# Optimization experiments

Hardware: AMD Instinct MI355X
Metric: run time of the kernel (lower is better)

The kernel has to match this reference:

```python
import jax, jax.numpy as jnp
from jax import lax
import numpy as np

GRID = 64
MAP = 15000.0
SCALE = MAP / GRID  # 234.375
R = int(1100 / SCALE)  # 4
SIGMA = 1.5
C = 16
B = 768
N_KILL = 49152
N_TRAIL = 393216

TOWERS = np.array([(8955, 8510), (9767, 10113), (11134, 11207), (11593, 11669), (13052, 12612), (12611, 13084), (5846, 6396), (5048, 4812), (3651, 3696), (3210, 3217), (2177, 1807), (1748, 2270), (4318, 13875), (981, 10441), (7943, 13411), (1512, 6699), (1169, 4287), (1172, 3583), (10481, 13650), (11275, 13657), (11275, 13663), (13866, 4505), (10504, 1029), (13327, 8226), (13624, 10572), (6919, 1483), (13599, 11319), (4281, 1253), (3468, 1230), (13594, 11319)], dtype=np.float32)

# ---- static buffers (numpy, computed once at import) ----
_tg = np.clip((TOWERS / SCALE).astype(np.int64), 0, GRID - 1)
TX, TY = _tg[:, 0], _tg[:, 1]
_xs = np.arange(GRID)
# per-tower coverage disc on the full canvas: equivalent to clipped range_mask placement
DISC = (((_xs[None, None, :] - TX[:, None, None]) ** 2 + (_xs[None, :, None] - TY[:, None, None]) ** 2) <= R * R).astype(np.float32)  # [30, H, W]
_ks = int(2 * 4 * SIGMA + 1)
if _ks % 2 == 0:
    _ks += 1
_x = (np.arange(_ks) - _ks // 2).astype(np.float32)
_k1 = np.exp(-_x ** 2 / (2 * SIGMA ** 2))
_k2 = np.outer(_k1, _k1)
_k2 = _k2 / _k2.sum()
KERNEL = np.broadcast_to(_k2, (C, 1, _ks, _ks)).astype(np.float32).copy()  # depthwise OIHW
PAD = _ks // 2
DRAG_X, DRAG_Y = int(10000.0 / SCALE), int(5000.0 / SCALE)   # (42, 21)
BARON_X, BARON_Y = int(5000.0 / SCALE), int(10000.0 / SCALE)  # (21, 42)


def _to_grid(coords):
    return jnp.clip((coords / SCALE).astype(jnp.int32), 0, GRID - 1)


def setup_inputs() -> dict:
    key = jax.random.key(0)
    ks = jax.random.split(key, 10)
    return {
        "player_coords": jax.random.uniform(ks[0], (N_TRAIL, 2), jnp.float32) * MAP,
        "player_vals": jax.random.uniform(ks[1], (N_TRAIL,), jnp.float32),
        "dead_towers_mask": jax.random.uniform(ks[2], (B, 30), jnp.float32),
        "kill_coords": jax.random.uniform(ks[3], (N_KILL, 2), jnp.float32) * MAP,
        "kill_vals": jax.random.uniform(ks[4], (N_KILL,), jnp.float32),
        "obj_status": jax.random.uniform(ks[5], (B, 2), jnp.float32),
        "player_b_idx": jax.random.randint(ks[6], (N_TRAIL,), 0, B, jnp.int32),
        "player_channels": jax.random.randint(ks[7], (N_TRAIL,), 0, 10, jnp.int32),
        "kill_teams": jax.random.randint(ks[8], (N_KILL,), 0, 2, jnp.int32),
        "kill_b_idx": jax.random.randint(ks[9], (N_KILL,), 0, B, jnp.int32),
    }


def reference(player_coords, player_vals, dead_towers_mask, kill_coords, kill_vals, obj_status, player_b_idx, player_channels, kill_teams, kill_b_idx):
    b = dead_towers_mask.shape[0]
    dead = dead_towers_mask > 0.5          # [B, 30]
    alive_f = (~dead).astype(jnp.float32)
    dead_f = dead.astype(jnp.float32)

    # channels 0/1: alive/dead tower markers (idempotent set -> scatter-max)
    ch0 = jnp.zeros((b, GRID, GRID), jnp.float32).at[:, TY, TX].max(alive_f)
    ch1 = jnp.zeros((b, GRID, GRID), jnp.float32).at[:, TY, TX].max(dead_f)

    # channel 2: max of binary range discs over alive towers == any-coverage indicator
    cov = alive_f @ jnp.asarray(DISC).reshape(30, -1)  # [B, H*W]
    ch2 = (cov > 0).astype(jnp.float32).reshape(b, GRID, GRID)

    # channel 3: objective markers
    ch3 = (jnp.zeros((b, GRID, GRID), jnp.float32)
           .at[:, DRAG_Y, DRAG_X].set((obj_status[:, 0] > 0.5).astype(jnp.float32))
           .at[:, BARON_Y, BARON_X].set((obj_status[:, 1] > 0.5).astype(jnp.float32)))

    canvas = jnp.concatenate(
        [ch0[:, None], ch1[:, None], ch2[:, None], ch3[:, None],
         jnp.zeros((b, C - 4, GRID, GRID), jnp.float32)], axis=1)  # [B, 16, H, W]

    # kill events: scatter-add into channels 4 + team
    kg = _to_grid(kill_coords)
    canvas = canvas.at[kill_b_idx, 4 + kill_teams, kg[:, 1], kg[:, 0]].add(kill_vals)

    # player trails: scatter-add into channels 6 + player_channel
    pg = _to_grid(player_coords)
    canvas = canvas.at[player_b_idx, 6 + player_channels, pg[:, 1], pg[:, 0]].add(player_vals)

    # depthwise gaussian blur
    blurred = lax.conv_general_dilated(
        canvas, jnp.asarray(KERNEL),
        window_strides=(1, 1), padding=[(PAD, PAD), (PAD, PAD)],
        feature_group_count=C,
        dimension_numbers=("NCHW", "OIHW", "NCHW"))
    return blurred
```

## Files before the change

### kernel.cpp

```cpp
#include <hip/hip_runtime.h>
#include <string.h>

#define GRID    64
#define BATCH   768
#define C       16
#define NT      30
#define N_KILL  49152
#define N_TRAIL 393216
#define CELLS   4096
#define IMG     (C * CELLS)
#define SCALE   234.375f
#define NSC     12
#define NIMG    (BATCH * NSC)
#define CAPI    128
#define STR     65
#define ROWS    76
#define HWORDS  (ROWS * STR)

__device__ constexpr int TXc[NT] = {38,41,47,49,55,53,24,21,15,13, 9, 7,18, 4,33, 6, 4, 5,44,48,48,59,44,56,58,29,58,18,14,58};
__device__ constexpr int TYc[NT] = {36,43,47,49,53,55,27,20,15,13, 7, 9,59,44,57,28,18,15,58,58,58,19, 4,35,45, 6,48, 5, 5,48};

__device__ constexpr float W13[13] = {
    8.92216e-05f, 1.02820e-03f, 7.59741e-03f, 3.59943e-02f, 1.09341e-01f,
    2.12968e-01f, 2.65964e-01f, 2.12968e-01f, 1.09341e-01f, 3.59943e-02f,
    7.59741e-03f, 1.02820e-03f, 8.92216e-05f};

__global__ __launch_bounds__(256) void zero_counts(unsigned* __restrict__ counts) {
    const int gid = blockIdx.x * 256 + threadIdx.x;
    if (gid < NIMG) counts[gid] = 0;
}

__global__ __launch_bounds__(256) void bin_points(
    const float* __restrict__ kc, const float* __restrict__ kv,
    const int*   __restrict__ kt, const int*   __restrict__ kb,
    const float* __restrict__ pc, const float* __restrict__ pv,
    const int*   __restrict__ pb, const int*   __restrict__ pch,
    unsigned* __restrict__ counts, unsigned* __restrict__ recs)
{
    const int gid = blockIdx.x * 256 + threadIdx.x;
    int img, gx, gy; float val;
    if (gid < N_KILL) {
        const int i = gid;
        const float2 xy = ((const float2*)kc)[i];
        gx = min(max((int)(xy.x / SCALE), 0), GRID - 1);
        gy = min(max((int)(xy.y / SCALE), 0), GRID - 1);
        val = kv[i];
        img = kb[i] * NSC + kt[i];
    } else {
        const int i = gid - N_KILL;
        const float2 xy = ((const float2*)pc)[i];
        gx = min(max((int)(xy.x / SCALE), 0), GRID - 1);
        gy = min(max((int)(xy.y / SCALE), 0), GRID - 1);
        val = pv[i];
        img = pb[i] * NSC + 2 + pch[i];
    }
    _Float16 h = (_Float16)val;
    unsigned short us;
    memcpy(&us, &h, 2);
    const unsigned rec = ((unsigned)(gy * GRID + gx) << 16) | (unsigned)us;
    const unsigned slot = atomicAdd(&counts[img], 1u);
    if (slot < CAPI) recs[(size_t)img * CAPI + slot] = rec;
}

template<bool BINS>
__global__ __launch_bounds__(256) void fused_blur(
    const float* __restrict__ dead_mask,
    const float* __restrict__ obj_status,
    const unsigned* __restrict__ counts,
    const unsigned* __restrict__ recs,
    const float* canvas,
    float* __restrict__ out)
{
    const int t  = threadIdx.x;
    const int bc = blockIdx.x;
    const int b  = bc >> 4;
    const int c  = bc & 15;
    const size_t base = (size_t)bc * CELLS;
    const int u = t & 63, q = t >> 6;

    __shared__ __align__(16) float s_h[HWORDS];
    __shared__ unsigned s_recs[CAPI];
    __shared__ float s_w[13];
    __shared__ float s_alive[NT];

    const bool sparse = (c != 2) && (BINS || c < 4);

    int n = 0;
    if (sparse) {
        if (c >= 4) {
            const int img = b * NSC + (c - 4);
            if (t < CAPI) s_recs[t] = recs[(size_t)img * CAPI + t];
            n = min((int)counts[img], CAPI);
        } else {
            if (t < 32) {
                int gx, gy; unsigned hbits = 0;
                if (t < NT) {
                    gx = TXc[t]; gy = TYc[t];
                    if (c != 3) {
                        const float a  = (dead_mask[b * NT + t] > 0.5f) ? 0.f : 1.f;
                        float v;
                        if (c == 0) {
                            v = (t == 20 || t == 29) ? 0.f
                              : (t == 19) ? fmaxf(a, (dead_mask[b*NT+20] > 0.5f) ? 0.f : 1.f)
                              : (t == 26) ? fmaxf(a, (dead_mask[b*NT+29] > 0.5f) ? 0.f : 1.f)
                              : a;
                        } else {
                            const float d = 1.f - a;
                            v = (t == 20 || t == 29) ? 0.f
                              : (t == 19) ? fmaxf(d, (dead_mask[b*NT+20] > 0.5f) ? 1.f : 0.f)
                              : (t == 26) ? fmaxf(d, (dead_mask[b*NT+29] > 0.5f) ? 1.f : 0.f)
                              : d;
                        }
                        hbits = (v > 0.5f) ? 0x3C00u : 0u;
                    }
                } else {
                    gx = (t == NT) ? 42 : 21;
                    gy = (t == NT) ? 21 : 42;
                    if (c == 3)
                        hbits = (obj_status[b * 2 + (t - NT)] > 0.5f) ? 0x3C00u : 0u;
                }
                s_recs[t] = ((unsigned)(gy * GRID + gx) << 16) | hbits;
            }
            n = 32;
        }
    } else if (c == 2) {
        if (t < NT) s_alive[t] = (dead_mask[b * NT + t] > 0.5f) ? 0.0f : 1.0f;
    }
    if (t < 13) s_w[t] = W13[t];

    {
        float4* z4 = (float4*)s_h;
        const float4 z = make_float4(0.f, 0.f, 0.f, 0.f);
        #pragma unroll
        for (int i = 0; i < 5; ++i) {
            const int idx = i * 256 + t;
            if (idx < HWORDS / 4) z4[idx] = z;
        }
    }
    __syncthreads();

    if (sparse) {
        const int ntaps = n * 13;
        for (int k0 = 0; k0 < ntaps; k0 += 256) {
            const int k = k0 + t;
            int i = (int)((unsigned)k / 13u);
            const int dd = k - i * 13;
            const bool valid = (k < ntaps);
            if (i > n - 1) i = n - 1;

            const unsigned rec = (n > 0) ? s_recs[i] : 0u;
            const int gx = (int)((rec >> 16) & 63u);
            const int gy = (int)(rec >> 22);
            const unsigned short us = (unsigned short)(rec & 0xFFFFu);
            _Float16 h;
            memcpy(&h, &us, 2);
            const float val = (float)h;

            const int   xl = gx - 6 + dd;
            if (valid && (unsigned)xl < 64u && val != 0.f)
                atomicAdd(&s_h[(6 + gy) * STR + xl], s_w[dd] * val);
        }
    } else {
        float w28[28];
        if (c == 2) {
            unsigned long long mask = 0ULL;
            #pragma unroll
            for (int i = 0; i < NT; ++i) {
                const int dy  = u - TYc[i];
                const int ady = dy < 0 ? -dy : dy;
                if (ady <= 4 && s_alive[i] > 0.0f) {
                    const int hw = (ady == 0) ? 4 : (ady <= 2) ? 3 : (ady == 3) ? 2 : 0;
                    int lo = TXc[i] - hw; if (lo < 0)  lo = 0;
                    int hi = TXc[i] + hw; if (hi > 63) hi = 63;
                    mask |= (((1ULL << (hi - lo + 1)) - 1ULL) << lo);
                }
            }
            #pragma unroll
            for (int k = 0; k < 28; ++k) {
                const int col = 16 * q - 6 + k;
                w28[k] = ((unsigned)col < 64u) ? (float)((mask >> col) & 1ULL) : 0.f;
            }
        } else {
            #pragma unroll
            for (int k = 0; k < 28; ++k) {
                const int col = 16 * q - 6 + k;
                w28[k] = ((unsigned)col < 64u) ? canvas[base + u * GRID + col] : 0.f;
            }
        }
        #pragma unroll
        for (int j = 0; j < 16; ++j) {
            float acc = 0.f;
            #pragma unroll
            for (int d = 0; d < 13; ++d) acc = fmaf(W13[d], w28[j + d], acc);
            s_h[(6 + u) * STR + 16 * q + j] = acc;
        }
    }
    __syncthreads();

    float v[28];
    #pragma unroll
    for (int k = 0; k < 28; ++k) v[k] = s_h[(16 * q + k) * STR + u];
    #pragma unroll
    for (int j = 0; j < 16; ++j) {
        float acc = 0.f;
        #pragma unroll
        for (int d = 0; d < 13; ++d) acc = fmaf(W13[d], v[j + d], acc);
        out[base + (16 * q + j) * GRID + u] = acc;
    }
}

__global__ __launch_bounds__(256) void zero12(float* __restrict__ out) {
    const int j = blockIdx.x;
    const int b = j / NSC, ch = 4 + j % NSC;
    float4* p = (float4*)(out + (size_t)(b * C + ch) * CELLS);
    #pragma unroll
    for (int k = 0; k < 4; ++k) p[k * 256 + threadIdx.x] = make_float4(0.f,0.f,0.f,0.f);
}

__global__ __launch_bounds__(256) void scatter_global(
    const float* __restrict__ kc, const float* __restrict__ kv,
    const int*   __restrict__ kt, const int*   __restrict__ kb,
    const float* __restrict__ pc, const float* __restrict__ pv,
    const int*   __restrict__ pb, const int*   __restrict__ pch,
    float* __restrict__ out)
{
    const int gid = blockIdx.x * 256 + threadIdx.x;
    if (gid < N_KILL) {
        const int i = gid;
        const int gx = min(max((int)(kc[2*i]   / SCALE), 0), GRID - 1);
        const int gy = min(max((int)(kc[2*i+1] / SCALE), 0), GRID - 1);
        atomicAdd(out + (size_t)kb[i]*IMG + (4+kt[i])*CELLS + gy*GRID + gx, kv[i]);
    } else {
        const int i = gid - N_KILL;
        const int gx = min(max((int)(pc[2*i]   / SCALE), 0), GRID - 1);
        const int gy = min(max((int)(pc[2*i+1] / SCALE), 0), GRID - 1);
        atomicAdd(out + (size_t)pb[i]*IMG + (6+pch[i])*CELLS + gy*GRID + gx, pv[i]);
    }
}

extern "C" void kernel_launch(void* const* d_in, const int* in_sizes, int n_in,
                              void* d_out, int out_size, void* d_ws, size_t ws_size,
                              hipStream_t stream)
{
    const float* player_coords = (const float*)d_in[0];
    const float* player_vals   = (const float*)d_in[1];
    const float* dead_mask     = (const float*)d_in[2];
    const float* kill_coords   = (const float*)d_in[3];
    const float* kill_vals     = (const float*)d_in[4];
    const float* obj_status    = (const float*)d_in[5];
    const int*   player_b      = (const int*)d_in[6];
    const int*   player_ch     = (const int*)d_in[7];
    const int*   kill_teams    = (const int*)d_in[8];
    const int*   kill_b        = (const int*)d_in[9];
    float* out = (float*)d_out;

    const size_t counts_bytes = (size_t)NIMG * sizeof(unsigned);
    const size_t recs_bytes   = (size_t)NIMG * CAPI * sizeof(unsigned);
    const int n_scatter_blocks = (N_KILL + N_TRAIL) / 256;

    if (ws_size >= counts_bytes + recs_bytes) {
        unsigned* counts = (unsigned*)d_ws;
        unsigned* recs   = (unsigned*)((char*)d_ws + counts_bytes);
        zero_counts<<<(NIMG + 255) / 256, 256, 0, stream>>>(counts);
        bin_points<<<n_scatter_blocks, 256, 0, stream>>>(
            kill_coords, kill_vals, kill_teams, kill_b,
            player_coords, player_vals, player_b, player_ch,
            counts, recs);
        fused_blur<true><<<BATCH * C, 256, 0, stream>>>(
            dead_mask, obj_status, counts, recs, nullptr, out);
    } else {
        zero12<<<NIMG, 256, 0, stream>>>(out);
        scatter_global<<<n_scatter_blocks, 256, 0, stream>>>(
            kill_coords, kill_vals, kill_teams, kill_b,
            player_coords, player_vals, player_b, player_ch, out);
        fused_blur<false><<<BATCH * C, 256, 0, stream>>>(
            dead_mask, obj_status, nullptr, nullptr, out, out);
    }
}
```

Measured before the change: 101.9 us.

## Fuse zero, bin and blur into one cooperative persistent kernel with grid syncs

Replaces the three-kernel sequence (zero counts, bin points, blur) with a single cooperative persistent kernel. It uses grid-wide syncs between the phases and loops over images with a grid-stride. The aim is to remove two kernel launch boundaries and their drain/fill gaps. In exchange it adds host-side occupancy queries on each call, grid.sync overhead, and a grid limited to resident blocks, which may cost blur throughput; if the cooperative launch fails it falls back to the old path.

```diff
diff --git a/kernel.cpp b/kernel.cpp
--- a/kernel.cpp
+++ b/kernel.cpp
@@ -1,5 +1,8 @@
 #include <hip/hip_runtime.h>
+#include <hip/hip_cooperative_groups.h>
 #include <string.h>
+
+namespace cg = cooperative_groups;
 
 #define GRID    64
 #define BATCH   768
@@ -7,6 +10,7 @@
 #define NT      30
 #define N_KILL  49152
 #define N_TRAIL 393216
+#define NPTS    (N_KILL + N_TRAIL)
 #define CELLS   4096
 #define IMG     (C * CELLS)
 #define SCALE   234.375f
@@ -25,63 +29,24 @@
     2.12968e-01f, 2.65964e-01f, 2.12968e-01f, 1.09341e-01f, 3.59943e-02f,
     7.59741e-03f, 1.02820e-03f, 8.92216e-05f};
 
-__global__ __launch_bounds__(256) void zero_counts(unsigned* __restrict__ counts) {
-    const int gid = blockIdx.x * 256 + threadIdx.x;
-    if (gid < NIMG) counts[gid] = 0;
-}
-
-__global__ __launch_bounds__(256) void bin_points(
-    const float* __restrict__ kc, const float* __restrict__ kv,
-    const int*   __restrict__ kt, const int*   __restrict__ kb,
-    const float* __restrict__ pc, const float* __restrict__ pv,
-    const int*   __restrict__ pb, const int*   __restrict__ pch,
-    unsigned* __restrict__ counts, unsigned* __restrict__ recs)
-{
-    const int gid = blockIdx.x * 256 + threadIdx.x;
-    int img, gx, gy; float val;
-    if (gid < N_KILL) {
-        const int i = gid;
-        const float2 xy = ((const float2*)kc)[i];
-        gx = min(max((int)(xy.x / SCALE), 0), GRID - 1);
-        gy = min(max((int)(xy.y / SCALE), 0), GRID - 1);
-        val = kv[i];
-        img = kb[i] * NSC + kt[i];
-    } else {
-        const int i = gid - N_KILL;
-        const float2 xy = ((const float2*)pc)[i];
-        gx = min(max((int)(xy.x / SCALE), 0), GRID - 1);
-        gy = min(max((int)(xy.y / SCALE), 0), GRID - 1);
-        val = pv[i];
-        img = pb[i] * NSC + 2 + pch[i];
-    }
-    _Float16 h = (_Float16)val;
-    unsigned short us;
-    memcpy(&us, &h, 2);
-    const unsigned rec = ((unsigned)(gy * GRID + gx) << 16) | (unsigned)us;
-    const unsigned slot = atomicAdd(&counts[img], 1u);
-    if (slot < CAPI) recs[(size_t)img * CAPI + slot] = rec;
-}
-
 template<bool BINS>
-__global__ __launch_bounds__(256) void fused_blur(
+__device__ __forceinline__ void blur_image(
+    int bc,
     const float* __restrict__ dead_mask,
     const float* __restrict__ obj_status,
     const unsigned* __restrict__ counts,
     const unsigned* __restrict__ recs,
     const float* canvas,
-    float* __restrict__ out)
-{
-    const int t  = threadIdx.x;
-    const int bc = blockIdx.x;
-    const int b  = bc >> 4;
-    const int c  = bc & 15;
+    float* __restrict__ out,
+    float* s_h, unsigned* s_recs, float* s_w, float* s_alive)
+{
+    const int t = threadIdx.x;
+    const int b = bc >> 4;
+    const int c = bc & 15;
     const size_t base = (size_t)bc * CELLS;
     const int u = t & 63, q = t >> 6;
 
-    __shared__ __align__(16) float s_h[HWORDS];
-    __shared__ unsigned s_recs[CAPI];
-    __shared__ float s_w[13];
-    __shared__ float s_alive[NT];
+    __syncthreads();
 
     const bool sparse = (c != 2) && (BINS || c < 4);
 
@@ -97,7 +62,7 @@
                 if (t < NT) {
                     gx = TXc[t]; gy = TYc[t];
                     if (c != 3) {
-                        const float a  = (dead_mask[b * NT + t] > 0.5f) ? 0.f : 1.f;
+                        const float a = (dead_mask[b * NT + t] > 0.5f) ? 0.f : 1.f;
                         float v;
                         if (c == 0) {
                             v = (t == 20 || t == 29) ? 0.f
@@ -156,7 +121,7 @@
             memcpy(&h, &us, 2);
             const float val = (float)h;
 
-            const int   xl = gx - 6 + dd;
+            const int xl = gx - 6 + dd;
             if (valid && (unsigned)xl < 64u && val != 0.f)
                 atomicAdd(&s_h[(6 + gy) * STR + xl], s_w[dd] * val);
         }
@@ -209,6 +174,102 @@
     }
 }
 
+__device__ __forceinline__ void bin_one(
+    int p,
+    const float* __restrict__ kc, const float* __restrict__ kv,
+    const int*   __restrict__ kt, const int*   __restrict__ kb,
+    const float* __restrict__ pc, const float* __restrict__ pv,
+    const int*   __restrict__ pb, const int*   __restrict__ pch,
+    unsigned* __restrict__ counts, unsigned* __restrict__ recs)
+{
+    int img, gx, gy; float val;
+    if (p < N_KILL) {
+        const float2 xy = ((const float2*)kc)[p];
+        gx = min(max((int)(xy.x / SCALE), 0), GRID - 1);
+        gy = min(max((int)(xy.y / SCALE), 0), GRID - 1);
+        val = kv[p];
+        img = kb[p] * NSC + kt[p];
+    } else {
+        const int i = p - N_KILL;
+        const float2 xy = ((const float2*)pc)[i];
+        gx = min(max((int)(xy.x / SCALE), 0), GRID - 1);
+        gy = min(max((int)(xy.y / SCALE), 0), GRID - 1);
+        val = pv[i];
+        img = pb[i] * NSC + 2 + pch[i];
+    }
+    _Float16 h = (_Float16)val;
+    unsigned short us;
+    memcpy(&us, &h, 2);
+    const unsigned rec = ((unsigned)(gy * GRID + gx) << 16) | (unsigned)us;
+    const unsigned slot = atomicAdd(&counts[img], 1u);
+    if (slot < CAPI) recs[(size_t)img * CAPI + slot] = rec;
+}
+
+__global__ __launch_bounds__(256, 6) void mega(
+    const float* __restrict__ kc, const float* __restrict__ kv,
+    const int*   __restrict__ kt, const int*   __restrict__ kb,
+    const float* __restrict__ pc, const float* __restrict__ pv,
+    const int*   __restrict__ pb, const int*   __restrict__ pch,
+    const float* __restrict__ dead_mask,
+    const float* __restrict__ obj_status,
+    unsigned* __restrict__ counts, unsigned* __restrict__ recs,
+    float* __restrict__ out)
+{
+    __shared__ __align__(16) float s_h[HWORDS];
+    __shared__ unsigned s_recs[CAPI];
+    __shared__ float s_w[13];
+    __shared__ float s_alive[NT];
+
+    cg::grid_group grid = cg::this_grid();
+    const int gid    = blockIdx.x * 256 + threadIdx.x;
+    const int stride = gridDim.x * 256;
+
+    for (int i = gid; i < NIMG; i += stride) counts[i] = 0;
+    grid.sync();
+
+    for (int p = gid; p < NPTS; p += stride)
+        bin_one(p, kc, kv, kt, kb, pc, pv, pb, pch, counts, recs);
+    grid.sync();
+
+    for (int bc = blockIdx.x; bc < BATCH * C; bc += gridDim.x)
+        blur_image<true>(bc, dead_mask, obj_status, counts, recs, nullptr, out,
+                         s_h, s_recs, s_w, s_alive);
+}
+
+__global__ __launch_bounds__(256) void zero_counts(unsigned* __restrict__ counts) {
+    const int gid = blockIdx.x * 256 + threadIdx.x;
+    if (gid < NIMG) counts[gid] = 0;
+}
+
+__global__ __launch_bounds__(256) void bin_points(
+    const float* __restrict__ kc, const float* __restrict__ kv,
+    const int*   __restrict__ kt, const int*   __restrict__ kb,
+    const float* __restrict__ pc, const float* __restrict__ pv,
+    const int*   __restrict__ pb, const int*   __restrict__ pch,
+    unsigned* __restrict__ counts, unsigned* __restrict__ recs)
+{
+    const int gid = blockIdx.x * 256 + threadIdx.x;
+    if (gid < NPTS)
+        bin_one(gid, kc, kv, kt, kb, pc, pv, pb, pch, counts, recs);
+}
+
+template<bool BINS>
+__global__ __launch_bounds__(256) void fused_blur_k(
+    const float* __restrict__ dead_mask,
+    const float* __restrict__ obj_status,
+    const unsigned* __restrict__ counts,
+    const unsigned* __restrict__ recs,
+    const float* canvas,
+    float* __restrict__ out)
+{
+    __shared__ __align__(16) float s_h[HWORDS];
+    __shared__ unsigned s_recs[CAPI];
+    __shared__ float s_w[13];
+    __shared__ float s_alive[NT];
+    blur_image<BINS>(blockIdx.x, dead_mask, obj_status, counts, recs, canvas, out,
+                     s_h, s_recs, s_w, s_alive);
+}
+
 __global__ __launch_bounds__(256) void zero12(float* __restrict__ out) {
     const int j = blockIdx.x;
     const int b = j / NSC, ch = 4 + j % NSC;
@@ -242,38 +303,55 @@
                               void* d_out, int out_size, void* d_ws, size_t ws_size,
                               hipStream_t stream)
 {
-    const float* player_coords = (const float*)d_in[0];
-    const float* player_vals   = (const float*)d_in[1];
-    const float* dead_mask     = (const float*)d_in[2];
-    const float* kill_coords   = (const float*)d_in[3];
-    const float* kill_vals     = (const float*)d_in[4];
-    const float* obj_status    = (const float*)d_in[5];
-    const int*   player_b      = (const int*)d_in[6];
-    const int*   player_ch     = (const int*)d_in[7];
-    const int*   kill_teams    = (const int*)d_in[8];
-    const int*   kill_b        = (const int*)d_in[9];
+    const float* pc  = (const float*)d_in[0];
+    const float* pv  = (const float*)d_in[1];
+    const float* dm  = (const float*)d_in[2];
+    const float* kc  = (const float*)d_in[3];
+    const float* kv  = (const float*)d_in[4];
+    const float* obj = (const float*)d_in[5];
+    const int*   pb  = (const int*)d_in[6];
+    const int*   pch = (const int*)d_in[7];
+    const int*   kt  = (const int*)d_in[8];
+    const int*   kb  = (const int*)d_in[9];
     float* out = (float*)d_out;
 
     const size_t counts_bytes = (size_t)NIMG * sizeof(unsigned);
     const size_t recs_bytes   = (size_t)NIMG * CAPI * sizeof(unsigned);
-    const int n_scatter_blocks = (N_KILL + N_TRAIL) / 256;
+    const int n_scatter_blocks = (NPTS + 255) / 256;
 
     if (ws_size >= counts_bytes + recs_bytes) {
         unsigned* counts = (unsigned*)d_ws;
         unsigned* recs   = (unsigned*)((char*)d_ws + counts_bytes);
-        zero_counts<<<(NIMG + 255) / 256, 256, 0, stream>>>(counts);
-        bin_points<<<n_scatter_blocks, 256, 0, stream>>>(
-            kill_coords, kill_vals, kill_teams, kill_b,
-            player_coords, player_vals, player_b, player_ch,
-            counts, recs);
-        fused_blur<true><<<BATCH * C, 256, 0, stream>>>(
-            dead_mask, obj_status, counts, recs, nullptr, out);
+
+        int nb = 0, cus = 0;
+        (void)hipOccupancyMaxActiveBlocksPerMultiprocessor(&nb, (const void*)mega, 256, 0);
+        (void)hipDeviceGetAttribute(&cus, hipDeviceAttributeMultiprocessorCount, 0);
+        long G = (long)nb * (long)cus;
+        if (G > BATCH * C) G = BATCH * C;
+
+        bool done = false;
+        if (G >= 256) {
+            void* args[] = {(void*)&kc, (void*)&kv, (void*)&kt, (void*)&kb,
+                            (void*)&pc, (void*)&pv, (void*)&pb, (void*)&pch,
+                            (void*)&dm, (void*)&obj,
+                            (void*)&counts, (void*)&recs, (void*)&out};
+            hipError_t e = hipLaunchCooperativeKernel((const void*)mega,
+                                                      dim3((unsigned)G), dim3(256),
+                                                      args, 0, stream);
+            done = (e == hipSuccess);
+        }
+        if (!done) {
+            zero_counts<<<(NIMG + 255) / 256, 256, 0, stream>>>(counts);
+            bin_points<<<n_scatter_blocks, 256, 0, stream>>>(
+                kc, kv, kt, kb, pc, pv, pb, pch, counts, recs);
+            fused_blur_k<true><<<BATCH * C, 256, 0, stream>>>(
+                dm, obj, counts, recs, nullptr, out);
+        }
     } else {
         zero12<<<NIMG, 256, 0, stream>>>(out);
         scatter_global<<<n_scatter_blocks, 256, 0, stream>>>(
-            kill_coords, kill_vals, kill_teams, kill_b,
-            player_coords, player_vals, player_b, player_ch, out);
-        fused_blur<false><<<BATCH * C, 256, 0, stream>>>(
-            dead_mask, obj_status, nullptr, nullptr, out, out);
-    }
-}
+            kc, kv, kt, kb, pc, pv, pb, pch, out);
+        fused_blur_k<false><<<BATCH * C, 256, 0, stream>>>(
+            dm, obj, nullptr, nullptr, out, out);
+    }
+}
```

New measurement: 268.8 us. +163.7%, slower.
